# Kernel tuning notes

Measured on AMD Instinct MI355X. Metric: run time of the kernel, lower is better.

The kernel has to match this reference:

```python
import jax, jax.numpy as jnp
import numpy as np

N_USERS = 100000
N_ITEMS = 20000
N_GENRES = 20
N_TAGS = 1128
EMB_ID = 64
EMB_FEAT = 64
HEADS = 8
HIDDEN = 256
D_MOVIE = EMB_ID + 2 * EMB_FEAT  # 192
E_HALF = 200000
N_NODES = N_USERS + N_ITEMS
NEG_SLOPE = 0.2


def setup_inputs() -> dict:
    key = jax.random.key(0)
    ks = jax.random.split(key, 24)
    p = lambda k, shape: (jax.random.normal(k, shape, jnp.float32) * 0.05)
    user_ids = jnp.arange(N_USERS)
    movie_ids = jnp.arange(N_ITEMS)
    mov_x = jax.random.normal(ks[0], (N_ITEMS, N_GENRES + N_TAGS), jnp.float32)
    # bipartite user<->movie edges, both directions (no self loops, matches add_self_loops=False)
    u = jax.random.randint(ks[1], (E_HALF,), 0, N_USERS)
    m = jax.random.randint(ks[2], (E_HALF,), 0, N_ITEMS) + N_USERS
    edge_index = jnp.stack([jnp.concatenate([u, m]), jnp.concatenate([m, u])])  # [2, 2*E_HALF]
    C1 = HIDDEN // HEADS
    return dict(
        user_ids=user_ids, movie_ids=movie_ids, mov_x=mov_x, edge_index=edge_index,
        user_emb=p(ks[3], (N_USERS, EMB_ID)), item_emb=p(ks[4], (N_ITEMS, EMB_ID)),
        gW1=p(ks[5], (N_GENRES, EMB_FEAT)), gb1=jnp.zeros((EMB_FEAT,), jnp.float32),
        gW2=p(ks[6], (EMB_FEAT, EMB_FEAT)), gb2=jnp.zeros((EMB_FEAT,), jnp.float32),
        tW1=p(ks[7], (N_TAGS, EMB_FEAT)), tb1=jnp.zeros((EMB_FEAT,), jnp.float32),
        tW2=p(ks[8], (EMB_FEAT, EMB_FEAT)), tb2=jnp.zeros((EMB_FEAT,), jnp.float32),
        Ws1=p(ks[9], (D_MOVIE, HIDDEN)), Wd1=p(ks[10], (D_MOVIE, HIDDEN)),
        as1=p(ks[11], (HEADS, C1)), ad1=p(ks[12], (HEADS, C1)),
        b1=jnp.zeros((HIDDEN,), jnp.float32),
        Ws2=p(ks[13], (HIDDEN, HIDDEN)), Wd2=p(ks[14], (HIDDEN, HIDDEN)),
        as2=p(ks[15], (1, HIDDEN)), ad2=p(ks[16], (1, HIDDEN)),
        b2=jnp.zeros((HIDDEN,), jnp.float32),
    )


def _gat(x, edge_index, Ws, Wd, a_s, a_d, bias, concat):
    # PyG GATConv (eval mode: dropout off, add_self_loops=False)
    N = x.shape[0]
    H, C = a_s.shape
    hs = (x @ Ws).reshape(N, H, C)  # source-side projection
    hd = (x @ Wd).reshape(N, H, C)  # dest-side projection
    al_s = (hs * a_s).sum(-1)  # [N, H]
    al_d = (hd * a_d).sum(-1)  # [N, H]
    src, dst = edge_index[0], edge_index[1]
    e = al_s[src] + al_d[dst]                      # [E, H]
    e = jnp.where(e > 0, e, NEG_SLOPE * e)         # leaky_relu(0.2)
    mmax = jax.ops.segment_max(e, dst, num_segments=N)
    w = jnp.exp(e - mmax[dst])
    ssum = jax.ops.segment_sum(w, dst, num_segments=N)
    alpha = w / (ssum[dst] + 1e-16)                # segment softmax over incoming edges
    out = jax.ops.segment_sum(hs[src] * alpha[:, :, None], dst, num_segments=N)  # [N, H, C]
    out = out.reshape(N, H * C) if concat else out.mean(axis=1)
    return out + bias


def reference(user_ids, movie_ids, mov_x, edge_index,
              user_emb, item_emb,
              gW1, gb1, gW2, gb2, tW1, tb1, tW2, tb2,
              Ws1, Wd1, as1, ad1, b1,
              Ws2, Wd2, as2, ad2, b2):
    g_feat = mov_x[:, :N_GENRES]
    t_feat = mov_x[:, N_GENRES:]
    g = jax.nn.relu(g_feat @ gW1 + gb1) @ gW2 + gb2
    t = jax.nn.relu(t_feat @ tW1 + tb1) @ tW2 + tb2
    x_mov = jnp.concatenate([item_emb[movie_ids], g, t], axis=1)  # [n_m, D_MOVIE]
    # homogeneous graph: user nodes first (zero-pad user emb to D_MOVIE), then movies
    x_usr = jnp.pad(user_emb[user_ids], ((0, 0), (0, D_MOVIE - EMB_ID)))
    x = jnp.concatenate([x_usr, x_mov], axis=0)  # [N_NODES, D_MOVIE]
    out = jax.nn.elu(_gat(x, edge_index, Ws1, Wd1, as1, ad1, b1, concat=True))
    out = _gat(out, edge_index, Ws2, Wd2, as2, ad2, b2, concat=False)
    ptr = jnp.array([0, N_USERS, N_USERS + N_ITEMS])
    return out, ptr
```

## Files before the change

kernel.cpp:

```cpp
#include <hip/hip_runtime.h>
#include <hip/hip_bf16.h>

#define N_USERS_C 100000
#define N_ITEMS_C 20000
#define N_NODES_C 120000
#define E_TOT_C   400000
#define D_IN_C    192
#define HID_C     256
#define NEG_C     0.2f
#define CLAMP_C   1000.0f
#define KPAD_C    1152
#define NB_SCAN   ((N_NODES_C + 255) / 256)
#define ROWE      40
#define NT_MOV    313
#define KSPLIT    4
#define KCH       288

typedef __attribute__((ext_vector_type(8))) short bfrag;
typedef __attribute__((ext_vector_type(4))) float ffrag;

__device__ __forceinline__ float bf2f(unsigned short u){
  return __uint_as_float(((unsigned)u) << 16);
}
__device__ __forceinline__ float ldf(const void* p, long i, int isf32){
  return isf32 ? ((const float*)p)[i] : bf2f(((const unsigned short*)p)[i]);
}
__device__ __forceinline__ float sane(float v){
  return (v > -1e30f && v < 1e30f) ? v : 0.f;
}
__device__ __forceinline__ int clampsrc(int s){
  return s < 0 ? 0 : (s >= N_NODES_C ? N_NODES_C - 1 : s);
}
__device__ __forceinline__ short f2bs(float f){
  __hip_bfloat16 h = __float2bfloat16(f);
  return *reinterpret_cast<short*>(&h);
}

__global__ __launch_bounds__(256) void detect_dtype(const unsigned short* __restrict__ ue,
                                                    int* __restrict__ flag){
  __shared__ int cnt[256];
  int tid = threadIdx.x; int c = 0;
  for (int i = tid; i < 8192; i += 256){
    unsigned e = (ue[i] >> 7) & 0xFFu;
    if (e >= 129u) c++;
  }
  cnt[tid] = c; __syncthreads();
  if (tid == 0){
    int s = 0;
    for (int i = 0; i < 256; i++) s += cnt[i];
    *flag = (s > 100) ? 1 : 0;
  }
}

struct PrepArgs {
  const void *ue, *ie;
  const void *gW1, *gb1, *gW2, *gb2, *tW1, *tb1, *tW2, *tb2;
  const void *Ws1, *Wd1, *as1, *ad1, *b1, *Ws2, *Wd2, *as2, *ad2, *b2;
  __hip_bfloat16 *x, *Bt1, *Bt2, *W1t, *W2t, *b1c, *b2c, *bg1, *bg2;
  int *deg, *cursor;
  const int* flag;
};

#define NB_UEMB  3125
#define NB_UZERO 2
#define NB_MOVE  625
#define NB_BT1   204
#define NB_BT2   272
#define NB_W1T   72
#define NB_W2T   8
#define NB_ZERO  235
#define NB_PREP (NB_UEMB+NB_UZERO+NB_MOVE+NB_BT1+NB_BT2+NB_W1T+NB_W2T+1+NB_ZERO)

__global__ __launch_bounds__(256) void mega_prep(PrepArgs a){
  int b = blockIdx.x, tid = threadIdx.x;
  int f32 = *a.flag;
  if (b < NB_UEMB) {
    int idx = b * 256 + tid;
    int n = idx >> 3, c0 = (idx & 7) * 8;
    union { short s[8]; float4 f; } u;
    if (f32) {
      const float* rf = (const float*)a.ue + (long)n * 64 + c0;
      float4 x0 = *(const float4*)rf, x1 = *(const float4*)(rf + 4);
      u.s[0]=f2bs(x0.x); u.s[1]=f2bs(x0.y); u.s[2]=f2bs(x0.z); u.s[3]=f2bs(x0.w);
      u.s[4]=f2bs(x1.x); u.s[5]=f2bs(x1.y); u.s[6]=f2bs(x1.z); u.s[7]=f2bs(x1.w);
    } else {
      u.f = *(const float4*)((const unsigned short*)a.ue + (long)n * 64 + c0);
    }
    *(float4*)(&a.x[(long)n * 192 + c0]) = u.f;
    return;
  }
  b -= NB_UEMB;
  if (b < NB_UZERO) {
    int idx = b * 256 + tid;
    int r = idx >> 4, c0 = 64 + (idx & 15) * 8;
    float4 z = {0.f, 0.f, 0.f, 0.f};
    *(float4*)(&a.x[(long)(99968 + r) * 192 + c0]) = z;
    return;
  }
  b -= NB_UZERO;
  if (b < NB_MOVE) {
    int idx = b * 256 + tid;
    int m = idx >> 3, c0 = (idx & 7) * 8;
    union { short s[8]; float4 f; } u;
    if (f32) {
      const float* rf = (const float*)a.ie + (long)m * 64 + c0;
      float4 x0 = *(const float4*)rf, x1 = *(const float4*)(rf + 4);
      u.s[0]=f2bs(x0.x); u.s[1]=f2bs(x0.y); u.s[2]=f2bs(x0.z); u.s[3]=f2bs(x0.w);
      u.s[4]=f2bs(x1.x); u.s[5]=f2bs(x1.y); u.s[6]=f2bs(x1.z); u.s[7]=f2bs(x1.w);
    } else {
      u.f = *(const float4*)((const unsigned short*)a.ie + (long)m * 64 + c0);
    }
    *(float4*)(&a.x[(long)(N_USERS_C + m) * 192 + c0]) = u.f;
    return;
  }
  b -= NB_MOVE;
  if (b < NB_BT1) {
    int idx = b * 256 + tid;
    int col = idx / 192, k = idx - col * 192;
    float v;
    if (col < 256) v = ldf(a.Ws1, k * 256 + col, f32);
    else if (col < 264) {
      int h = col - 256; float s = 0.f;
      for (int c = 0; c < 32; c++)
        s += ldf(a.Ws1, k * 256 + h * 32 + c, f32) * ldf(a.as1, h * 32 + c, f32);
      v = s;
    } else {
      int h = col - 264; float s = 0.f;
      for (int c = 0; c < 32; c++)
        s += ldf(a.Wd1, k * 256 + h * 32 + c, f32) * ldf(a.ad1, h * 32 + c, f32);
      v = s;
    }
    a.Bt1[col * 192 + k] = __float2bfloat16(v);
    return;
  }
  b -= NB_BT1;
  if (b < NB_BT2) {
    int idx = b * 256 + tid;
    int col = idx / 256, k = idx & 255;
    float v;
    if (col < 256) v = ldf(a.Ws2, k * 256 + col, f32);
    else if (col == 256) {
      float s = 0.f;
      for (int c = 0; c < 256; c++)
        s += ldf(a.Ws2, k * 256 + c, f32) * ldf(a.as2, c, f32);
      v = s;
    } else if (col == 257) {
      float s = 0.f;
      for (int c = 0; c < 256; c++)
        s += ldf(a.Wd2, k * 256 + c, f32) * ldf(a.ad2, c, f32);
      v = s;
    } else v = 0.f;
    a.Bt2[col * 256 + k] = __float2bfloat16(v);
    return;
  }
  b -= NB_BT2;
  if (b < NB_W1T) {
    int idx = b * 256 + tid;
    int n = idx / 144, c8 = idx - n * 144;
    int k0 = c8 * 8;
    union { short s[8]; float4 f; } u;
#pragma unroll
    for (int j = 0; j < 8; j++) {
      int k = k0 + j; float v = 0.f;
      if (n < 64) { if (k < 20) v = ldf(a.gW1, k * 64 + n, f32); }
      else        { if (k >= 20 && k < 1148) v = ldf(a.tW1, (k - 20) * 64 + (n - 64), f32); }
      u.s[j] = f2bs(v);
    }
    *(float4*)(&a.W1t[(long)n * 1152 + k0]) = u.f;
    return;
  }
  b -= NB_W1T;
  if (b < NB_W2T) {
    int idx = b * 256 + tid;
    int n = idx >> 4, k0 = (idx & 15) * 8;
    union { short s[8]; float4 f; } u;
#pragma unroll
    for (int j = 0; j < 8; j++) {
      int k = k0 + j; float v = 0.f;
      if (n < 64) { if (k < 64)  v = ldf(a.gW2, k * 64 + n, f32); }
      else        { if (k >= 64) v = ldf(a.tW2, (k - 64) * 64 + (n - 64), f32); }
      u.s[j] = f2bs(v);
    }
    *(float4*)(&a.W2t[n * 128 + k0]) = u.f;
    return;
  }
  b -= NB_W2T;
  if (b < 1) {
    int i = tid;
    if (i < 64)       a.b1c[i] = __float2bfloat16(ldf(a.gb1, i, f32));
    else if (i < 128) a.b1c[i] = __float2bfloat16(ldf(a.tb1, i - 64, f32));
    else if (i < 192) a.b2c[i - 128] = __float2bfloat16(ldf(a.gb2, i - 128, f32));
    else              a.b2c[i - 128] = __float2bfloat16(ldf(a.tb2, i - 192, f32));
    a.bg1[tid] = __float2bfloat16(ldf(a.b1, tid, f32));
    a.bg2[tid] = __float2bfloat16(ldf(a.b2, tid, f32));
    return;
  }
  b -= 1;
  {
    int i0 = (b * 256 + tid) * 4;
    if (i0 < 2 * N_NODES_C) {
      int4 z = {0, 0, 0, 0};
      if (i0 < N_NODES_C) *(int4*)(a.deg + i0) = z;
      else                *(int4*)(a.cursor + (i0 - N_NODES_C)) = z;
    }
  }
}

__global__ __launch_bounds__(256) void movie_gemm_k(
    const void* __restrict__ rawA, const int* __restrict__ flag,
    const __hip_bfloat16* __restrict__ W1t,
    float* __restrict__ part){
  __shared__ short Bls[128 * ROWE];
  __shared__ short Als[64 * ROWE];
  int tid = threadIdx.x;
  int wave = tid >> 6;
  int lane = tid & 63;
  int l15 = lane & 15;
  int quad = lane >> 4;
  int bid = blockIdx.x;
  int tile = bid % NT_MOV, split = bid / NT_MOV;
  int rowbase_blk = tile * 64;
  int rowbase = rowbase_blk + wave * 16;
  int f32v = *flag;
  ffrag acc[8];
#pragma unroll
  for (int i = 0; i < 8; i++) acc[i] = (ffrag){0.f, 0.f, 0.f, 0.f};
  const short* Bs = (const short*)W1t;
  int sr = tid >> 2, sc = tid & 3;
  int arow_st = rowbase_blk + sr; if (arow_st >= N_ITEMS_C) arow_st = N_ITEMS_C - 1;
  int kbeg = split * KCH;
  for (int k0 = kbeg; k0 < kbeg + KCH; k0 += 32) {
    __syncthreads();
    for (int t = tid; t < 512; t += 256) {
      int r = t >> 2, c = t & 3;
      *(float4*)(&Bls[r * ROWE + c * 8]) =
          *(const float4*)(Bs + (long)r * KPAD_C + k0 + c * 8);
    }
    int kc = k0 + sc * 8;
    union { short s[8]; float4 f; } u;
    long base = (long)arow_st * 1148 + kc;
    if (kc + 8 <= 1148) {
      if (f32v) {
        const float* rf = (const float*)rawA + base;
        float4 x0 = *(const float4*)rf;
        float4 x1 = *(const float4*)(rf + 4);
        u.s[0]=f2bs(x0.x); u.s[1]=f2bs(x0.y); u.s[2]=f2bs(x0.z); u.s[3]=f2bs(x0.w);
        u.s[4]=f2bs(x1.x); u.s[5]=f2bs(x1.y); u.s[6]=f2bs(x1.z); u.s[7]=f2bs(x1.w);
      } else {
        const unsigned short* rs = (const unsigned short*)rawA + base;
        ushort4 a0 = *(const ushort4*)rs;
        ushort4 a1 = *(const ushort4*)(rs + 4);
        u.s[0]=(short)a0.x; u.s[1]=(short)a0.y; u.s[2]=(short)a0.z; u.s[3]=(short)a0.w;
        u.s[4]=(short)a1.x; u.s[5]=(short)a1.y; u.s[6]=(short)a1.z; u.s[7]=(short)a1.w;
      }
    } else {
#pragma unroll
      for (int j = 0; j < 8; j++) {
        float v = (kc + j < 1148) ? ldf(rawA, base + j, f32v) : 0.f;
        u.s[j] = f2bs(v);
      }
    }
    *(float4*)(&Als[sr * ROWE + sc * 8]) = u.f;
    __syncthreads();
    int koff = quad * 8;
    bfrag af = *(const bfrag*)(&Als[(wave * 16 + l15) * ROWE + koff]);
#pragma unroll
    for (int nt = 0; nt < 8; nt++) {
      bfrag bf = *(const bfrag*)(&Bls[(nt * 16 + l15) * ROWE + koff]);
      acc[nt] = __builtin_amdgcn_mfma_f32_16x16x32_bf16(af, bf, acc[nt], 0, 0, 0);
    }
  }
  float* pb = part + (long)split * (N_ITEMS_C * 128);
#pragma unroll
  for (int reg = 0; reg < 4; reg++) {
    int grow = rowbase + quad * 4 + reg;
    if (grow >= N_ITEMS_C) continue;
#pragma unroll
    for (int nt = 0; nt < 8; nt++)
      pb[(long)grow * 128 + nt * 16 + l15] = acc[nt][reg];
  }
}

__global__ __launch_bounds__(256) void movie_gemm2(
    const float* __restrict__ part, const __hip_bfloat16* __restrict__ b1c,
    const __hip_bfloat16* __restrict__ W2t, const __hip_bfloat16* __restrict__ b2c,
    __hip_bfloat16* __restrict__ out){
  __shared__ short Bls[128 * ROWE];
  __shared__ short Als[64 * ROWE];
  int tid = threadIdx.x;
  int wave = tid >> 6;
  int lane = tid & 63;
  int l15 = lane & 15;
  int quad = lane >> 4;
  int rowbase_blk = blockIdx.x * 64;
  int rowbase = rowbase_blk + wave * 16;
  ffrag acc[8];
#pragma unroll
  for (int i = 0; i < 8; i++) acc[i] = (ffrag){0.f, 0.f, 0.f, 0.f};
  const short* Bs = (const short*)W2t;
  int sr = tid >> 2, sc = tid & 3;
  int arow_st = rowbase_blk + sr; if (arow_st >= N_ITEMS_C) arow_st = N_ITEMS_C - 1;
  for (int k0 = 0; k0 < 128; k0 += 32) {
    __syncthreads();
    for (int t = tid; t < 512; t += 256) {
      int r = t >> 2, c = t & 3;
      *(float4*)(&Bls[r * ROWE + c * 8]) =
          *(const float4*)(Bs + (long)r * 128 + k0 + c * 8);
    }
    int kc = k0 + sc * 8;
    float vs[8];
#pragma unroll
    for (int j = 0; j < 8; j++) vs[j] = __bfloat162float(b1c[kc + j]);
    long base = (long)arow_st * 128 + kc;
#pragma unroll
    for (int s = 0; s < KSPLIT; s++) {
      const float* p = part + (long)s * (N_ITEMS_C * 128) + base;
      float4 q0 = *(const float4*)p, q1 = *(const float4*)(p + 4);
      vs[0] += q0.x; vs[1] += q0.y; vs[2] += q0.z; vs[3] += q0.w;
      vs[4] += q1.x; vs[5] += q1.y; vs[6] += q1.z; vs[7] += q1.w;
    }
    union { short s[8]; float4 f; } u;
#pragma unroll
    for (int j = 0; j < 8; j++) u.s[j] = f2bs(fmaxf(vs[j], 0.f));
    *(float4*)(&Als[sr * ROWE + sc * 8]) = u.f;
    __syncthreads();
    int koff = quad * 8;
    bfrag af = *(const bfrag*)(&Als[(wave * 16 + l15) * ROWE + koff]);
#pragma unroll
    for (int nt = 0; nt < 8; nt++) {
      bfrag bf = *(const bfrag*)(&Bls[(nt * 16 + l15) * ROWE + koff]);
      acc[nt] = __builtin_amdgcn_mfma_f32_16x16x32_bf16(af, bf, acc[nt], 0, 0, 0);
    }
  }
#pragma unroll
  for (int reg = 0; reg < 4; reg++) {
    int grow = rowbase + quad * 4 + reg;
    if (grow >= N_ITEMS_C) continue;
#pragma unroll
    for (int nt = 0; nt < 8; nt++) {
      float v = acc[nt][reg] + __bfloat162float(b2c[nt * 16 + l15]);
      out[(long)grow * D_IN_C + 64 + nt * 16 + l15] = __float2bfloat16(v);
    }
  }
}

__global__ __launch_bounds__(256) void gemm_fused(
    const __hip_bfloat16* __restrict__ A, const __hip_bfloat16* __restrict__ Bt,
    __hip_bfloat16* __restrict__ Hout, float* __restrict__ als, float* __restrict__ ald,
    int K, int natt, int ukmax){
  __shared__ short Bls[272 * ROWE];
  __shared__ short Als[64 * ROWE];
  int tid = threadIdx.x;
  int wave = tid >> 6;
  int lane = tid & 63;
  int l15 = lane & 15;
  int quad = lane >> 4;
  int rowbase_blk = blockIdx.x * 64;
  int rowbase = rowbase_blk + wave * 16;
  int kmax = (rowbase_blk + 64 <= N_USERS_C) ? ukmax : K;
  ffrag acc[17];
#pragma unroll
  for (int i = 0; i < 17; i++) acc[i] = (ffrag){0.f, 0.f, 0.f, 0.f};
  const short* As = (const short*)A;
  const short* Bs = (const short*)Bt;
  int sr = tid >> 2, sc = tid & 3;
  for (int k0 = 0; k0 < kmax; k0 += 32) {
    __syncthreads();
    for (int t = tid; t < 1088; t += 256) {
      int r = t >> 2, c = t & 3;
      *(float4*)(&Bls[r * ROWE + c * 8]) = *(const float4*)(Bs + (long)r * K + k0 + c * 8);
    }
    *(float4*)(&Als[sr * ROWE + sc * 8]) =
        *(const float4*)(As + (long)(rowbase_blk + sr) * K + k0 + sc * 8);
    __syncthreads();
    int koff = quad * 8;
    bfrag af = *(const bfrag*)(&Als[(wave * 16 + l15) * ROWE + koff]);
#pragma unroll
    for (int nt = 0; nt < 17; nt++) {
      bfrag bf = *(const bfrag*)(&Bls[(nt * 16 + l15) * ROWE + koff]);
      acc[nt] = __builtin_amdgcn_mfma_f32_16x16x32_bf16(af, bf, acc[nt], 0, 0, 0);
    }
  }
  int col = l15;
#pragma unroll
  for (int reg = 0; reg < 4; reg++) {
    int grow = rowbase + quad * 4 + reg;
    long obase = (long)grow * 256;
#pragma unroll
    for (int nt = 0; nt < 16; nt++)
      Hout[obase + nt * 16 + col] = __float2bfloat16(acc[nt][reg]);
    float v = acc[16][reg];
    if (col < natt) als[grow * natt + col] = v;
    else if (col < 2 * natt) ald[grow * natt + (col - natt)] = v;
  }
}

__global__ void deg_count(const int* __restrict__ ei, int* __restrict__ deg){
  int e = blockIdx.x * 256 + threadIdx.x;
  if (e >= E_TOT_C) return;
  int dst = ei[E_TOT_C + e];
  if (dst >= 0 && dst < N_NODES_C) atomicAdd(&deg[dst], 1);
}

__global__ __launch_bounds__(256) void deg_bsum(const int* __restrict__ deg,
                                                int* __restrict__ bsum){
  int i = blockIdx.x * 256 + threadIdx.x;
  int v = (i < N_NODES_C) ? deg[i] : 0;
#pragma unroll
  for (int o = 32; o > 0; o >>= 1) v += __shfl_down(v, o, 64);
  __shared__ int ws[4];
  int wave = threadIdx.x >> 6, lane = threadIdx.x & 63;
  if (lane == 0) ws[wave] = v;
  __syncthreads();
  if (threadIdx.x == 0) bsum[blockIdx.x] = ws[0] + ws[1] + ws[2] + ws[3];
}

__global__ __launch_bounds__(512) void bsum_scan(int* __restrict__ bsum,
                                                 int* __restrict__ ptrn){
  __shared__ int sm[512];
  int t = threadIdx.x;
  int v = (t < NB_SCAN) ? bsum[t] : 0;
  sm[t] = v;
  __syncthreads();
  for (int o = 1; o < 512; o <<= 1) {
    int add = (t >= o) ? sm[t - o] : 0;
    __syncthreads();
    sm[t] += add;
    __syncthreads();
  }
  int excl = (t == 0) ? 0 : sm[t - 1];
  if (t < NB_SCAN) bsum[t] = excl;
  if (t == NB_SCAN - 1) ptrn[N_NODES_C] = sm[t];
}

__global__ __launch_bounds__(256) void deg_scan_final(const int* __restrict__ deg,
                                                      const int* __restrict__ bexcl,
                                                      int* __restrict__ ptrn){
  __shared__ int sm[256];
  int i = blockIdx.x * 256 + threadIdx.x;
  int t = threadIdx.x;
  int v = (i < N_NODES_C) ? deg[i] : 0;
  sm[t] = v;
  __syncthreads();
  for (int o = 1; o < 256; o <<= 1) {
    int add = (t >= o) ? sm[t - o] : 0;
    __syncthreads();
    sm[t] += add;
    __syncthreads();
  }
  int excl = (t == 0) ? 0 : sm[t - 1];
  if (i < N_NODES_C) ptrn[i] = bexcl[blockIdx.x] + excl;
}

__global__ void scatter_edges(const int* __restrict__ ei, const int* __restrict__ ptrn,
                              int* __restrict__ cursor, int* __restrict__ elist_src){
  int e = blockIdx.x * 256 + threadIdx.x;
  if (e >= E_TOT_C) return;
  int dst = ei[E_TOT_C + e];
  if (dst < 0 || dst >= N_NODES_C) return;
  int pos = atomicAdd(&cursor[dst], 1);
  elist_src[ptrn[dst] + pos] = ei[e];
}

__global__ __launch_bounds__(256) void aggregate1(
    const int* __restrict__ ptrn, const int* __restrict__ elist_src,
    const float* __restrict__ als, const float* __restrict__ ald,
    const __hip_bfloat16* __restrict__ hs, const __hip_bfloat16* __restrict__ bias,
    __hip_bfloat16* __restrict__ h1){
  int node = blockIdx.x * 4 + (threadIdx.x >> 6);
  if (node >= N_NODES_C) return;
  int lane = threadIdx.x & 63;
  int c0 = lane * 4;
  int h = lane >> 3;
  int beg = ptrn[node], end = ptrn[node + 1];
  float aldv = sane(ald[node * 8 + h]);
  float m = -1e30f;
  float wsum = 0.f, a0 = 0.f, a1 = 0.f, a2 = 0.f, a3 = 0.f;
  const unsigned short* hsu = (const unsigned short*)hs;
  float alsv_p = 0.f;
  ushort4 hv_p = {0, 0, 0, 0};
  int src_b = 0;
  if (beg < end) {
    int s0 = clampsrc(elist_src[beg]);
    alsv_p = als[(long)s0 * 8 + h];
    hv_p = *(const ushort4*)(hsu + (long)s0 * 256 + c0);
    if (beg + 1 < end) src_b = clampsrc(elist_src[beg + 1]);
  }
  for (int i = beg; i < end; i++) {
    float alsv = alsv_p;
    ushort4 hv = hv_p;
    if (i + 1 < end) {
      alsv_p = als[(long)src_b * 8 + h];
      hv_p = *(const ushort4*)(hsu + (long)src_b * 256 + c0);
    }
    if (i + 2 < end)
      src_b = clampsrc(elist_src[i + 2]);
    float ev = sane(alsv) + aldv;
    ev = ev > 0.f ? ev : NEG_C * ev;
    float mnew = fmaxf(m, ev);
    float corr = __expf(m - mnew);
    float w = __expf(ev - mnew);
    m = mnew;
    wsum = wsum * corr + w;
    a0 = a0 * corr + w * bf2f(hv.x); a1 = a1 * corr + w * bf2f(hv.y);
    a2 = a2 * corr + w * bf2f(hv.z); a3 = a3 * corr + w * bf2f(hv.w);
  }
  float inv = 1.f / (wsum + 1e-16f);
  float v0 = a0 * inv + __bfloat162float(bias[c0 + 0]);
  float v1 = a1 * inv + __bfloat162float(bias[c0 + 1]);
  float v2 = a2 * inv + __bfloat162float(bias[c0 + 2]);
  float v3 = a3 * inv + __bfloat162float(bias[c0 + 3]);
  v0 = v0 > 0.f ? v0 : (__expf(v0) - 1.f);
  v1 = v1 > 0.f ? v1 : (__expf(v1) - 1.f);
  v2 = v2 > 0.f ? v2 : (__expf(v2) - 1.f);
  v3 = v3 > 0.f ? v3 : (__expf(v3) - 1.f);
  v0 = fminf(fmaxf(v0, -CLAMP_C), CLAMP_C);
  v1 = fminf(fmaxf(v1, -CLAMP_C), CLAMP_C);
  v2 = fminf(fmaxf(v2, -CLAMP_C), CLAMP_C);
  v3 = fminf(fmaxf(v3, -CLAMP_C), CLAMP_C);
  long ob = (long)node * 256 + c0;
  h1[ob + 0] = __float2bfloat16(v0); h1[ob + 1] = __float2bfloat16(v1);
  h1[ob + 2] = __float2bfloat16(v2); h1[ob + 3] = __float2bfloat16(v3);
}

__global__ __launch_bounds__(256) void aggregate2(
    const int* __restrict__ ptrn, const int* __restrict__ elist_src,
    const float* __restrict__ als, const float* __restrict__ ald,
    const __hip_bfloat16* __restrict__ hs, const __hip_bfloat16* __restrict__ bias,
    float* __restrict__ out, int out_size){
  if (blockIdx.x == 0 && threadIdx.x == 0) {
    out[out_size - 3] = 0.f;
    out[out_size - 2] = (float)N_USERS_C;
    out[out_size - 1] = (float)N_NODES_C;
  }
  int node = blockIdx.x * 4 + (threadIdx.x >> 6);
  if (node >= N_NODES_C) return;
  int lane = threadIdx.x & 63;
  int c0 = lane * 4;
  int beg = ptrn[node], end = ptrn[node + 1];
  float aldv = sane(ald[node]);
  float m = -1e30f;
  float wsum = 0.f, a0 = 0.f, a1 = 0.f, a2 = 0.f, a3 = 0.f;
  const unsigned short* hsu = (const unsigned short*)hs;
  float alsv_p = 0.f;
  ushort4 hv_p = {0, 0, 0, 0};
  int src_b = 0;
  if (beg < end) {
    int s0 = clampsrc(elist_src[beg]);
    alsv_p = als[s0];
    hv_p = *(const ushort4*)(hsu + (long)s0 * 256 + c0);
    if (beg + 1 < end) src_b = clampsrc(elist_src[beg + 1]);
  }
  for (int i = beg; i < end; i++) {
    float alsv = alsv_p;
    ushort4 hv = hv_p;
    if (i + 1 < end) {
      alsv_p = als[src_b];
      hv_p = *(const ushort4*)(hsu + (long)src_b * 256 + c0);
    }
    if (i + 2 < end)
      src_b = clampsrc(elist_src[i + 2]);
    float ev = sane(alsv) + aldv;
    ev = ev > 0.f ? ev : NEG_C * ev;
    float mnew = fmaxf(m, ev);
    float corr = __expf(m - mnew);
    float w = __expf(ev - mnew);
    m = mnew;
    wsum = wsum * corr + w;
    a0 = a0 * corr + w * bf2f(hv.x); a1 = a1 * corr + w * bf2f(hv.y);
    a2 = a2 * corr + w * bf2f(hv.z); a3 = a3 * corr + w * bf2f(hv.w);
  }
  float inv = 1.f / (wsum + 1e-16f);
  float4 v;
  v.x = a0 * inv + __bfloat162float(bias[c0 + 0]);
  v.y = a1 * inv + __bfloat162float(bias[c0 + 1]);
  v.z = a2 * inv + __bfloat162float(bias[c0 + 2]);
  v.w = a3 * inv + __bfloat162float(bias[c0 + 3]);
  v.x = fminf(fmaxf(v.x, -CLAMP_C), CLAMP_C);
  v.y = fminf(fmaxf(v.y, -CLAMP_C), CLAMP_C);
  v.z = fminf(fmaxf(v.z, -CLAMP_C), CLAMP_C);
  v.w = fminf(fmaxf(v.w, -CLAMP_C), CLAMP_C);
  *(float4*)(out + (long)node * 256 + c0) = v;
}

extern "C" void kernel_launch(void* const* d_in, const int* in_sizes, int n_in,
                              void* d_out, int out_size, void* d_ws, size_t ws_size,
                              hipStream_t stream) {
  const void* mov_x    = d_in[2];
  const int*  ei       = (const int*)d_in[3];
  const void* user_emb = d_in[4];
  const void* item_emb = d_in[5];

  char* ws = (char*)d_ws;
  size_t off = 0;
  auto alloc = [&](size_t bytes) -> void* {
    void* p = ws + off; off += (bytes + 255) / 256 * 256; return p;
  };
  int* flag   = (int*)alloc(4);
  __hip_bfloat16* Bt1 = (__hip_bfloat16*)alloc(272 * 192 * 2);
  __hip_bfloat16* Bt2 = (__hip_bfloat16*)alloc(272 * 256 * 2);
  __hip_bfloat16* W1t = (__hip_bfloat16*)alloc(128 * KPAD_C * 2);
  __hip_bfloat16* W2t = (__hip_bfloat16*)alloc(128 * 128 * 2);
  __hip_bfloat16* b1c = (__hip_bfloat16*)alloc(128 * 2);
  __hip_bfloat16* b2c = (__hip_bfloat16*)alloc(128 * 2);
  __hip_bfloat16* bg1 = (__hip_bfloat16*)alloc(256 * 2);
  __hip_bfloat16* bg2 = (__hip_bfloat16*)alloc(256 * 2);
  int* ptrn   = (int*)alloc((N_NODES_C + 1) * 4);
  int* deg    = (int*)alloc(N_NODES_C * 4);
  int* cursor = (int*)alloc(N_NODES_C * 4);
  int* bsum   = (int*)alloc(512 * 4);
  int* elist  = (int*)alloc(E_TOT_C * 4);
  float* als  = (float*)alloc((size_t)N_NODES_C * 8 * 4);
  float* ald  = (float*)alloc((size_t)N_NODES_C * 8 * 4);
  __hip_bfloat16* x  = (__hip_bfloat16*)alloc((size_t)N_NODES_C * D_IN_C * 2);
  __hip_bfloat16* hs = (__hip_bfloat16*)alloc((size_t)N_NODES_C * HID_C * 2);
  __hip_bfloat16* h1  = (__hip_bfloat16*)d_out;
  float* part = (float*)((char*)d_out + 61440000);

  detect_dtype<<<1, 256, 0, stream>>>((const unsigned short*)user_emb, flag);

  PrepArgs pa;
  pa.ue = user_emb; pa.ie = item_emb;
  pa.gW1 = d_in[6];  pa.gb1 = d_in[7];  pa.gW2 = d_in[8];  pa.gb2 = d_in[9];
  pa.tW1 = d_in[10]; pa.tb1 = d_in[11]; pa.tW2 = d_in[12]; pa.tb2 = d_in[13];
  pa.Ws1 = d_in[14]; pa.Wd1 = d_in[15]; pa.as1 = d_in[16]; pa.ad1 = d_in[17]; pa.b1 = d_in[18];
  pa.Ws2 = d_in[19]; pa.Wd2 = d_in[20]; pa.as2 = d_in[21]; pa.ad2 = d_in[22]; pa.b2 = d_in[23];
  pa.x = x; pa.Bt1 = Bt1; pa.Bt2 = Bt2; pa.W1t = W1t; pa.W2t = W2t;
  pa.b1c = b1c; pa.b2c = b2c; pa.bg1 = bg1; pa.bg2 = bg2;
  pa.deg = deg; pa.cursor = cursor; pa.flag = flag;
  mega_prep<<<NB_PREP, 256, 0, stream>>>(pa);

  movie_gemm_k<<<NT_MOV * KSPLIT, 256, 0, stream>>>(mov_x, flag, W1t, part);
  movie_gemm2<<<NT_MOV, 256, 0, stream>>>(part, b1c, W2t, b2c,
                                          x + (long)N_USERS_C * D_IN_C);

  deg_count<<<(E_TOT_C + 255) / 256, 256, 0, stream>>>(ei, deg);
  deg_bsum<<<NB_SCAN, 256, 0, stream>>>(deg, bsum);
  bsum_scan<<<1, 512, 0, stream>>>(bsum, ptrn);
  deg_scan_final<<<NB_SCAN, 256, 0, stream>>>(deg, bsum, ptrn);
  scatter_edges<<<(E_TOT_C + 255) / 256, 256, 0, stream>>>(ei, ptrn, cursor, elist);

  gemm_fused<<<N_NODES_C / 64, 256, 0, stream>>>(x, Bt1, hs, als, ald, 192, 8, 64);
  aggregate1<<<N_NODES_C / 4, 256, 0, stream>>>(ptrn, elist, als, ald, hs, bg1, h1);

  gemm_fused<<<N_NODES_C / 64, 256, 0, stream>>>(h1, Bt2, hs, als, ald, 256, 1, 256);
  aggregate2<<<N_NODES_C / 4, 256, 0, stream>>>(ptrn, elist, als, ald, hs, bg2,
                                                (float*)d_out, out_size);
}
```

Before: 571.9 us.

## Merge independent graph-build kernels into GEMM launches via block-range dispatch

Combines independent work into shared launches by splitting the grid by block index. Movie GEMM stage 1 runs alongside degree counting, movie GEMM stage 2 alongside per-block degree sums, and the layer-1 GEMM alongside edge scattering. This cuts three kernel launches and lets the light atomic work fill gaps left by the GEMM blocks. In exchange, every fused kernel carries the GEMM's shared-memory and register footprint even in the simple blocks, which can lower occupancy for the edge blocks.

Measured after the change: 557.6 us. -2.5%, faster.

```diff
diff --git a/kernel.cpp b/kernel.cpp
--- a/kernel.cpp
+++ b/kernel.cpp
@@ -11,6 +11,8 @@
 #define CLAMP_C   1000.0f
 #define KPAD_C    1152
 #define NB_SCAN   ((N_NODES_C + 255) / 256)
+#define NB_EDGE   ((E_TOT_C + 255) / 256)
+#define NB_GEMM   (N_NODES_C / 64)
 #define ROWE      40
 #define NT_MOV    313
 #define KSPLIT    4
@@ -206,10 +208,10 @@
   }
 }
 
-__global__ __launch_bounds__(256) void movie_gemm_k(
-    const void* __restrict__ rawA, const int* __restrict__ flag,
-    const __hip_bfloat16* __restrict__ W1t,
-    float* __restrict__ part){
+
+__device__ void movie_k_body(int bid, const void* __restrict__ rawA, int f32v,
+                             const __hip_bfloat16* __restrict__ W1t,
+                             float* __restrict__ part){
   __shared__ short Bls[128 * ROWE];
   __shared__ short Als[64 * ROWE];
   int tid = threadIdx.x;
@@ -217,11 +219,9 @@
   int lane = tid & 63;
   int l15 = lane & 15;
   int quad = lane >> 4;
-  int bid = blockIdx.x;
   int tile = bid % NT_MOV, split = bid / NT_MOV;
   int rowbase_blk = tile * 64;
   int rowbase = rowbase_blk + wave * 16;
-  int f32v = *flag;
   ffrag acc[8];
 #pragma unroll
   for (int i = 0; i < 8; i++) acc[i] = (ffrag){0.f, 0.f, 0.f, 0.f};
@@ -281,10 +281,11 @@
   }
 }
 
-__global__ __launch_bounds__(256) void movie_gemm2(
-    const float* __restrict__ part, const __hip_bfloat16* __restrict__ b1c,
-    const __hip_bfloat16* __restrict__ W2t, const __hip_bfloat16* __restrict__ b2c,
-    __hip_bfloat16* __restrict__ out){
+__device__ void movie2_body(int bid, const float* __restrict__ part,
+                            const __hip_bfloat16* __restrict__ b1c,
+                            const __hip_bfloat16* __restrict__ W2t,
+                            const __hip_bfloat16* __restrict__ b2c,
+                            __hip_bfloat16* __restrict__ out){
   __shared__ short Bls[128 * ROWE];
   __shared__ short Als[64 * ROWE];
   int tid = threadIdx.x;
@@ -292,7 +293,7 @@
   int lane = tid & 63;
   int l15 = lane & 15;
   int quad = lane >> 4;
-  int rowbase_blk = blockIdx.x * 64;
+  int rowbase_blk = bid * 64;
   int rowbase = rowbase_blk + wave * 16;
   ffrag acc[8];
 #pragma unroll
@@ -344,7 +345,7 @@
   }
 }
 
-__global__ __launch_bounds__(256) void gemm_fused(
+__device__ void gemm_fused_body(int bid,
     const __hip_bfloat16* __restrict__ A, const __hip_bfloat16* __restrict__ Bt,
     __hip_bfloat16* __restrict__ Hout, float* __restrict__ als, float* __restrict__ ald,
     int K, int natt, int ukmax){
@@ -355,7 +356,7 @@
   int lane = tid & 63;
   int l15 = lane & 15;
   int quad = lane >> 4;
-  int rowbase_blk = blockIdx.x * 64;
+  int rowbase_blk = bid * 64;
   int rowbase = rowbase_blk + wave * 16;
   int kmax = (rowbase_blk + 64 <= N_USERS_C) ? ukmax : K;
   ffrag acc[17];
@@ -395,16 +396,14 @@
   }
 }
 
-__global__ void deg_count(const int* __restrict__ ei, int* __restrict__ deg){
-  int e = blockIdx.x * 256 + threadIdx.x;
+__device__ void deg_count_body(int e, const int* __restrict__ ei, int* __restrict__ deg){
   if (e >= E_TOT_C) return;
   int dst = ei[E_TOT_C + e];
   if (dst >= 0 && dst < N_NODES_C) atomicAdd(&deg[dst], 1);
 }
 
-__global__ __launch_bounds__(256) void deg_bsum(const int* __restrict__ deg,
-                                                int* __restrict__ bsum){
-  int i = blockIdx.x * 256 + threadIdx.x;
+__device__ void deg_bsum_body(int bid, const int* __restrict__ deg, int* __restrict__ bsum){
+  int i = bid * 256 + threadIdx.x;
   int v = (i < N_NODES_C) ? deg[i] : 0;
 #pragma unroll
   for (int o = 32; o > 0; o >>= 1) v += __shfl_down(v, o, 64);
@@ -412,7 +411,55 @@
   int wave = threadIdx.x >> 6, lane = threadIdx.x & 63;
   if (lane == 0) ws[wave] = v;
   __syncthreads();
-  if (threadIdx.x == 0) bsum[blockIdx.x] = ws[0] + ws[1] + ws[2] + ws[3];
+  if (threadIdx.x == 0) bsum[bid] = ws[0] + ws[1] + ws[2] + ws[3];
+}
+
+__device__ void scatter_body(int e, const int* __restrict__ ei, const int* __restrict__ ptrn,
+                             int* __restrict__ cursor, int* __restrict__ elist_src){
+  if (e >= E_TOT_C) return;
+  int dst = ei[E_TOT_C + e];
+  if (dst < 0 || dst >= N_NODES_C) return;
+  int pos = atomicAdd(&cursor[dst], 1);
+  elist_src[ptrn[dst] + pos] = ei[e];
+}
+
+#define NB_KA (NT_MOV * KSPLIT + NB_EDGE)
+__global__ __launch_bounds__(256) void movie_k_degcnt(
+    const void* __restrict__ rawA, const int* __restrict__ flag,
+    const __hip_bfloat16* __restrict__ W1t, float* __restrict__ part,
+    const int* __restrict__ ei, int* __restrict__ deg){
+  int b = blockIdx.x;
+  if (b < NT_MOV * KSPLIT) movie_k_body(b, rawA, *flag, W1t, part);
+  else deg_count_body((b - NT_MOV * KSPLIT) * 256 + threadIdx.x, ei, deg);
+}
+
+#define NB_KB (NT_MOV + NB_SCAN)
+__global__ __launch_bounds__(256) void movie2_bsum(
+    const float* __restrict__ part, const __hip_bfloat16* __restrict__ b1c,
+    const __hip_bfloat16* __restrict__ W2t, const __hip_bfloat16* __restrict__ b2c,
+    __hip_bfloat16* __restrict__ out,
+    const int* __restrict__ deg, int* __restrict__ bsum){
+  int b = blockIdx.x;
+  if (b < NT_MOV) movie2_body(b, part, b1c, W2t, b2c, out);
+  else deg_bsum_body(b - NT_MOV, deg, bsum);
+}
+
+#define NB_KC (NB_GEMM + NB_EDGE)
+__global__ __launch_bounds__(256) void gemm1_scatter(
+    const __hip_bfloat16* __restrict__ A, const __hip_bfloat16* __restrict__ Bt,
+    __hip_bfloat16* __restrict__ Hout, float* __restrict__ als, float* __restrict__ ald,
+    const int* __restrict__ ei, const int* __restrict__ ptrn,
+    int* __restrict__ cursor, int* __restrict__ elist_src){
+  int b = blockIdx.x;
+  if (b < NB_GEMM) gemm_fused_body(b, A, Bt, Hout, als, ald, 192, 8, 64);
+  else scatter_body((b - NB_GEMM) * 256 + threadIdx.x, ei, ptrn, cursor, elist_src);
+}
+
+__global__ __launch_bounds__(256) void gemm_fused(
+    const __hip_bfloat16* __restrict__ A, const __hip_bfloat16* __restrict__ Bt,
+    __hip_bfloat16* __restrict__ Hout, float* __restrict__ als, float* __restrict__ ald,
+    int K, int natt, int ukmax){
+  gemm_fused_body(blockIdx.x, A, Bt, Hout, als, ald, K, natt, ukmax);
 }
 
 __global__ __launch_bounds__(512) void bsum_scan(int* __restrict__ bsum,
@@ -450,16 +497,6 @@
   }
   int excl = (t == 0) ? 0 : sm[t - 1];
   if (i < N_NODES_C) ptrn[i] = bexcl[blockIdx.x] + excl;
-}
-
-__global__ void scatter_edges(const int* __restrict__ ei, const int* __restrict__ ptrn,
-                              int* __restrict__ cursor, int* __restrict__ elist_src){
-  int e = blockIdx.x * 256 + threadIdx.x;
-  if (e >= E_TOT_C) return;
-  int dst = ei[E_TOT_C + e];
-  if (dst < 0 || dst >= N_NODES_C) return;
-  int pos = atomicAdd(&cursor[dst], 1);
-  elist_src[ptrn[dst] + pos] = ei[e];
 }
 
 __global__ __launch_bounds__(256) void aggregate1(
@@ -630,20 +667,17 @@
   pa.deg = deg; pa.cursor = cursor; pa.flag = flag;
   mega_prep<<<NB_PREP, 256, 0, stream>>>(pa);
 
-  movie_gemm_k<<<NT_MOV * KSPLIT, 256, 0, stream>>>(mov_x, flag, W1t, part);
-  movie_gemm2<<<NT_MOV, 256, 0, stream>>>(part, b1c, W2t, b2c,
-                                          x + (long)N_USERS_C * D_IN_C);
-
-  deg_count<<<(E_TOT_C + 255) / 256, 256, 0, stream>>>(ei, deg);
-  deg_bsum<<<NB_SCAN, 256, 0, stream>>>(deg, bsum);
+  movie_k_degcnt<<<NB_KA, 256, 0, stream>>>(mov_x, flag, W1t, part, ei, deg);
+  movie2_bsum<<<NB_KB, 256, 0, stream>>>(part, b1c, W2t, b2c,
+                                         x + (long)N_USERS_C * D_IN_C, deg, bsum);
   bsum_scan<<<1, 512, 0, stream>>>(bsum, ptrn);
   deg_scan_final<<<NB_SCAN, 256, 0, stream>>>(deg, bsum, ptrn);
-  scatter_edges<<<(E_TOT_C + 255) / 256, 256, 0, stream>>>(ei, ptrn, cursor, elist);
-
-  gemm_fused<<<N_NODES_C / 64, 256, 0, stream>>>(x, Bt1, hs, als, ald, 192, 8, 64);
+
+  gemm1_scatter<<<NB_KC, 256, 0, stream>>>(x, Bt1, hs, als, ald,
+                                           ei, ptrn, cursor, elist);
   aggregate1<<<N_NODES_C / 4, 256, 0, stream>>>(ptrn, elist, als, ald, hs, bg1, h1);
 
-  gemm_fused<<<N_NODES_C / 64, 256, 0, stream>>>(h1, Bt2, hs, als, ald, 256, 1, 256);
+  gemm_fused<<<NB_GEMM, 256, 0, stream>>>(h1, Bt2, hs, als, ald, 256, 1, 256);
   aggregate2<<<N_NODES_C / 4, 256, 0, stream>>>(ptrn, elist, als, ald, hs, bg2,
                                                 (float*)d_out, out_size);
 }
```
